# Kernel tuning notes

Hardware: AMD Instinct MI355X
Metric: run time of the kernel (lower is better)

Reference implementation:

```python
import jax, jax.numpy as jnp
import numpy as np

E = 8_388_608  # total edges across batched graphs
G = 4096       # num_graphs


def setup_inputs() -> dict:
    key = jax.random.key(0)
    k1, k2, k3 = jax.random.split(key, 3)
    edge_scores = jax.random.normal(k1, (E,), dtype=jnp.float32)
    # edge_batch: sorted segment ids in [0, G), as in PyG batched graphs
    edge_batch = jnp.sort(jax.random.randint(k2, (E,), 0, G)).astype(jnp.int32)
    candidate_mask = jax.random.bernoulli(k3, 0.5, (E,))
    return {
        "edge_scores": edge_scores,
        "edge_batch": edge_batch,
        "candidate_mask": candidate_mask,
        "num_graphs": G,
        "k": 32,
    }


def reference(edge_scores, edge_batch, candidate_mask, num_graphs, k):
    """Segmented top-k edge selection (GFlowNetActor._select_topk_candidate_edges).

    Faithful fixed-shape formulation: candidate edges come in as a boolean mask
    over all E edges (the rollout builds cand_edges = nonzero(candidate_mask)),
    and the kept top-k-per-graph edges go out as a boolean pruned mask (the
    rollout scatters the returned indices back into pruned_mask). Also returns
    the score values gated by the pruned mask (differentiable output).
    """
    n = edge_scores.shape[0]
    neg_inf = jnp.finfo(jnp.float32).min
    # Non-candidates get -inf so they sort to the back of each segment
    s = jnp.where(candidate_mask, edge_scores.astype(jnp.float32), neg_inf)
    # Sort by score descending, then stably by segment id -> within each
    # graph edges appear in descending-score order (same double-argsort as torch)
    order_score = jnp.argsort(-s, stable=True)
    order_seg = jnp.argsort(edge_batch[order_score], stable=True)
    perm = order_score[order_seg]          # [E] edge ids sorted by (seg asc, score desc)
    seg_sorted = edge_batch[perm]          # [E]
    # Segment starts via bincount + exclusive cumsum
    counts = jnp.bincount(seg_sorted, length=num_graphs)
    start = jnp.concatenate(
        [jnp.zeros(1, jnp.int32), jnp.cumsum(counts)[:-1].astype(jnp.int32)]
    )
    rank = jnp.arange(n, dtype=jnp.int32) - start[seg_sorted]
    keep_sorted = (rank < k) & candidate_mask[perm]
    # Scatter keep flags back to original edge order
    pruned_mask = jnp.zeros(n, dtype=bool).at[perm].set(keep_sorted)
    pruned_scores = jnp.where(pruned_mask, edge_scores, jnp.float32(0.0))
    return pruned_mask, pruned_scores
```

## Files before the change

kernel.cpp:

```cpp
#include <hip/hip_runtime.h>
#include <stdint.h>

#define G_NUM 4096
#define BLOCK 256
#define CAP   3072
#define ACT   1152

typedef unsigned long long ull;

__device__ __forceinline__ unsigned int order_bits(float f) {
    unsigned int b = __float_as_uint(f);
    return (b & 0x80000000u) ? ~b : (b | 0x80000000u);
}
__device__ __forceinline__ float inv_order_bits(unsigned int ob) {
    return __uint_as_float((ob & 0x80000000u) ? (ob & 0x7FFFFFFFu) : ~ob);
}

__global__ void prep_kernel(const int* __restrict__ batch, int* __restrict__ start,
                            const unsigned int* __restrict__ mraw, int* __restrict__ flag,
                            int E) {
    if (blockIdx.x == 0 && threadIdx.x < 64) {
        int lane = threadIdx.x;
        bool allI = true, allF = true;
        for (int i = lane; i < 256; i += 64) {
            unsigned int w = mraw[i];
            if (w > 1u) allI = false;
            if (w != 0u && w != 0x3F800000u) allF = false;
        }
        allI = __all(allI);
        allF = __all(allF);
        if (lane == 0) *flag = allI ? 0 : (allF ? 1 : 2);
    }
    const int n4 = E >> 2;
    int i4 = blockIdx.x * blockDim.x + threadIdx.x;
    if (i4 >= n4) return;
    int4 b = ((const int4*)batch)[i4];
    int prev = __shfl_up(b.w, 1, 64);
    if ((threadIdx.x & 63) == 0) prev = (i4 == 0) ? -1 : batch[i4 * 4 - 1];
    const int e0 = i4 * 4;
    for (int g = prev + 1; g <= b.x; ++g) start[g] = e0;
    for (int g = b.x + 1; g <= b.y; ++g) start[g] = e0 + 1;
    for (int g = b.y + 1; g <= b.z; ++g) start[g] = e0 + 2;
    for (int g = b.z + 1; g <= b.w; ++g) start[g] = e0 + 3;
    if (i4 == n4 - 1) {
        int last = b.w, e = E & ~3;
        for (int t = 0; t < (E & 3); ++t) {
            int v = batch[e + t];
            for (int g = last + 1; g <= v; ++g) start[g] = e + t;
            last = v;
        }
        for (int g = last + 1; g <= G_NUM; ++g) start[g] = E;
    }
}

__device__ __forceinline__ void scan_select(
    unsigned int* hist, unsigned int* wtot, int kk,
    int* bsel_s, unsigned int* cgt_s, unsigned int* hsel_s, int* cnt2, int tid)
{
    unsigned int h = hist[tid];
    hist[tid] = 0u;
    unsigned int v = h;
    int lane = tid & 63, wv = tid >> 6;
    #pragma unroll
    for (int off = 1; off < 64; off <<= 1) {
        unsigned int o = __shfl_down(v, off, 64);
        if (lane + off < 64) v += o;
    }
    if (lane == 0) wtot[wv] = v;
    if (tid == 0) *cnt2 = 0;
    __syncthreads();
    unsigned int sfx = v;
    for (int w = wv + 1; w < 4; ++w) sfx += wtot[w];
    if ((unsigned)kk <= sfx && (unsigned)kk > sfx - h) {
        *bsel_s = tid; *cgt_s = sfx - h; *hsel_s = h;
    }
    __syncthreads();
}

__global__ __launch_bounds__(BLOCK) void topk_kernel(
    const float* __restrict__ scores, const void* __restrict__ maskp,
    const int* __restrict__ start, const int* __restrict__ kp,
    const int* __restrict__ flagp, float* __restrict__ out_mask,
    float* __restrict__ out_scores, int E)
{
    __shared__ unsigned int keys[CAP];
    __shared__ unsigned short act[2][ACT];
    __shared__ ull candb[CAP / 64];
    __shared__ unsigned int hist[256];
    __shared__ unsigned int wtot[4];
    __shared__ int cnt, cnt2, bsel_s, licut_s;
    __shared__ unsigned int cgt_s, hsel_s, P_s;

    const int g  = blockIdx.x;
    const int s0 = start[g];
    const int s1 = start[g + 1];
    const int len = s1 - s0;
    if (len <= 0) return;

    const int k     = *kp;
    const int mflag = *flagp;
    const int tid   = threadIdx.x;
    const int lane  = tid & 63;
    const int wv    = tid >> 6;

    auto getmask = [&](int i) -> bool {
        if (mflag == 2) return ((const unsigned char*)maskp)[i] != 0;
        if (mflag == 0) return ((const int*)maskp)[i] != 0;
        return ((const float*)maskp)[i] != 0.0f;
    };

    if (k <= 0) {
        for (int i = s0 + tid; i < s1; i += BLOCK) { out_mask[i] = 0.0f; out_scores[i] = 0.0f; }
        return;
    }

    hist[tid] = 0u;
    if (tid == 0) cnt = 0;
    __syncthreads();

    if (len <= CAP) {
        const int iters = (len + BLOCK - 1) / BLOCK;
        unsigned int wcnt = 0;
        for (int it = 0; it < iters; ++it) {
            int li = it * BLOCK + tid;
            bool c = false;
            if (li < len) {
                int i = s0 + li;
                c = getmask(i);
                unsigned kb = order_bits(scores[i]);
                keys[li] = kb;
                if (c) atomicAdd(&hist[kb >> 24], 1u);
            }
            ull bal = __ballot(c);
            if (lane == 0) {
                candb[it * 4 + wv] = bal;
                wcnt += __popcll(bal);
            }
        }
        if (lane == 0 && wcnt) atomicAdd(&cnt, (int)wcnt);
        __syncthreads();
        const int m = cnt;
        const bool keep_all = (m <= k);
        unsigned int P = 0u;
        int licut = 0;

        if (!keep_all) {
            unsigned int prefix = 0u;
            int kk = k;
            int ccnt = m;
            int compacted = -1;
            int alen = 0;

            for (int shift = 24; ; shift -= 8) {
                scan_select(hist, wtot, kk, &bsel_s, &cgt_s, &hsel_s, &cnt2, tid);
                const unsigned b   = (unsigned)bsel_s;
                const unsigned cgt = cgt_s;
                const int csel     = (int)hsel_s;

                if (csel <= ACT) {
                    if (compacted < 0) {
                        for (int it = 0; it < iters; ++it) {
                            int li = it * BLOCK + tid;
                            if (li >= len) break;
                            if (!((candb[li >> 6] >> (li & 63)) & 1)) continue;
                            unsigned key = keys[li];
                            if (shift < 24 && (key >> (shift + 8)) != (prefix >> (shift + 8))) continue;
                            if (((key >> shift) & 0xFFu) == b)
                                act[0][atomicAdd(&cnt2, 1)] = (unsigned short)li;
                        }
                        compacted = 0;
                    } else {
                        int src = compacted, dst = src ^ 1;
                        for (int j = tid; j < alen; j += BLOCK) {
                            unsigned short lj = act[src][j];
                            if (((keys[lj] >> shift) & 0xFFu) == b)
                                act[dst][atomicAdd(&cnt2, 1)] = lj;
                        }
                        compacted = dst;
                    }
                    alen = csel;
                }
                prefix |= b << shift;
                kk -= (int)cgt;
                ccnt = csel;
                __syncthreads();
                if (shift == 0 || (compacted >= 0 && ccnt <= 64)) break;

                if (compacted < 0) {
                    for (int it = 0; it < iters; ++it) {
                        int li = it * BLOCK + tid;
                        if (li >= len) break;
                        if (!((candb[li >> 6] >> (li & 63)) & 1)) continue;
                        unsigned key = keys[li];
                        if ((key >> shift) == (prefix >> shift))
                            atomicAdd(&hist[(key >> (shift - 8)) & 0xFFu], 1u);
                    }
                } else {
                    for (int j = tid; j < alen; j += BLOCK)
                        atomicAdd(&hist[(keys[act[compacted][j]] >> (shift - 8)) & 0xFFu], 1u);
                }
                __syncthreads();
            }

            if (tid == 0) { P_s = prefix; licut_s = 0x7FFFFFFF; }
            __syncthreads();
            if (compacted >= 0 && ccnt <= 64) {
                if (tid < 64) {
                    unsigned key = 0u; int li = 0x7FFFFFFF;
                    if (tid < ccnt) { li = act[compacted][tid]; key = keys[li]; }
                    int r = 0;
                    for (int j = 0; j < ccnt; ++j) {
                        unsigned kj = __shfl(key, j, 64);
                        int lj = __shfl(li, j, 64);
                        if (kj > key || (kj == key && lj < li)) r++;
                    }
                    if (tid < ccnt && r == kk - 1) { P_s = key; licut_s = li; }
                }
            } else if (compacted >= 0) {
                for (int e = tid; e < alen; e += BLOCK) {
                    int li = act[compacted][e];
                    if (keys[li] != prefix) continue;
                    int r = 0;
                    for (int j = 0; j < alen; ++j) {
                        int lj = act[compacted][j];
                        if (keys[lj] == prefix && lj < li) r++;
                    }
                    if (r == kk - 1) licut_s = li;
                }
            } else {
                for (int li = tid; li < len; li += BLOCK) {
                    if (!((candb[li >> 6] >> (li & 63)) & 1)) continue;
                    if (keys[li] != prefix) continue;
                    int r = 0;
                    for (int j = 0; j < len; ++j)
                        if (((candb[j >> 6] >> (j & 63)) & 1) && keys[j] == prefix && j < li) r++;
                    if (r == kk - 1) licut_s = li;
                }
            }
            __syncthreads();
            P = P_s; licut = licut_s;
        }

        for (int it = 0; it < iters; ++it) {
            int li = it * BLOCK + tid;
            if (li >= len) break;
            bool c = (candb[li >> 6] >> (li & 63)) & 1;
            unsigned key = keys[li];
            bool kept = c && (keep_all || key > P || (key == P && li <= licut));
            out_mask[s0 + li]   = kept ? 1.0f : 0.0f;
            out_scores[s0 + li] = kept ? inv_order_bits(key) : 0.0f;
        }
    } else {
        int lc = 0;
        for (int i = s0 + tid; i < s1; i += BLOCK)
            if (getmask(i)) lc++;
        atomicAdd(&cnt, lc);
        __syncthreads();
        const int m = cnt;
        const bool keep_all = (m <= k);
        ull pivot = 0ull;
        if (!keep_all) {
            ull prefix = 0ull;
            int kk = k;
            for (int shift = 56; shift >= 0; shift -= 8) {
                for (int i = s0 + tid; i < s1; i += BLOCK) {
                    if (!getmask(i)) continue;
                    ull key = ((ull)order_bits(scores[i]) << 32) |
                              (ull)(0xFFFFFFFFu - (unsigned)(i - s0));
                    if (shift == 56 || (key >> (shift + 8)) == (prefix >> (shift + 8)))
                        atomicAdd(&hist[(unsigned)((key >> shift) & 0xFFull)], 1u);
                }
                __syncthreads();
                scan_select(hist, wtot, kk, &bsel_s, &cgt_s, &hsel_s, &cnt2, tid);
                prefix |= ((ull)(unsigned)bsel_s) << shift;
                kk -= (int)cgt_s;
            }
            pivot = prefix;
        }
        for (int i = s0 + tid; i < s1; i += BLOCK) {
            bool c = getmask(i);
            float sc = 0.0f;
            bool kept = false;
            if (c) {
                sc = scores[i];
                ull key = ((ull)order_bits(sc) << 32) |
                          (ull)(0xFFFFFFFFu - (unsigned)(i - s0));
                kept = keep_all || (key >= pivot);
            }
            out_mask[i]   = kept ? 1.0f : 0.0f;
            out_scores[i] = kept ? sc : 0.0f;
        }
    }
}

extern "C" void kernel_launch(void* const* d_in, const int* in_sizes, int n_in,
                              void* d_out, int out_size, void* d_ws, size_t ws_size,
                              hipStream_t stream) {
    const float* scores = (const float*)d_in[0];
    const int*   batch  = (const int*)d_in[1];
    const void*  mask   = d_in[2];
    const int*   kp     = (const int*)d_in[4];
    const int    E      = in_sizes[0];

    float* out_mask   = (float*)d_out;
    float* out_scores = out_mask + E;

    int* flag  = (int*)d_ws;
    int* start = (int*)((char*)d_ws + 256);

    const int n4 = E >> 2;
    prep_kernel<<<(n4 + BLOCK - 1) / BLOCK, BLOCK, 0, stream>>>(
        batch, start, (const unsigned int*)mask, flag, E);
    topk_kernel<<<G_NUM, BLOCK, 0, stream>>>(scores, mask, start, kp, flag,
                                             out_mask, out_scores, E);
}
```

Before: 52.67 us.

## Keep per-thread keys in registers with vectorized loads and small-candidate rank select

The small-segment path now has each thread own 12 contiguous edges held in registers. Scores and masks are loaded as float4/int4/uint words on interior threads, which removes the shared-memory key array and compaction buffers. The radix select stops once at most 256 candidates remain, packs them into a shared list and ranks them all-pairs, with a binary-search fallback for ties. Outputs are written with vector stores. This cuts shared-memory footprint (raising occupancy) and memory transactions, at the cost of more registers and more complex boundary handling for unaligned segment edges.

Measured after the change: 57.80 us. 9.8% more time.

```diff
diff --git a/kernel.cpp b/kernel.cpp
--- a/kernel.cpp
+++ b/kernel.cpp
@@ -3,8 +3,9 @@
 
 #define G_NUM 4096
 #define BLOCK 256
-#define CAP   3072
-#define ACT   1152
+#define VPT   12
+#define CAP   (BLOCK * VPT - 3)
+#define CLS   256
 
 typedef unsigned long long ull;
 
@@ -83,11 +84,9 @@
     const int* __restrict__ flagp, float* __restrict__ out_mask,
     float* __restrict__ out_scores, int E)
 {
-    __shared__ unsigned int keys[CAP];
-    __shared__ unsigned short act[2][ACT];
-    __shared__ ull candb[CAP / 64];
     __shared__ unsigned int hist[256];
     __shared__ unsigned int wtot[4];
+    __shared__ ull cls[CLS];
     __shared__ int cnt, cnt2, bsel_s, licut_s;
     __shared__ unsigned int cgt_s, hsel_s, P_s;
 
@@ -100,8 +99,6 @@
     const int k     = *kp;
     const int mflag = *flagp;
     const int tid   = threadIdx.x;
-    const int lane  = tid & 63;
-    const int wv    = tid >> 6;
 
     auto getmask = [&](int i) -> bool {
         if (mflag == 2) return ((const unsigned char*)maskp)[i] != 0;
@@ -116,28 +113,79 @@
 
     hist[tid] = 0u;
     if (tid == 0) cnt = 0;
-    __syncthreads();
 
     if (len <= CAP) {
-        const int iters = (len + BLOCK - 1) / BLOCK;
-        unsigned int wcnt = 0;
-        for (int it = 0; it < iters; ++it) {
-            int li = it * BLOCK + tid;
-            bool c = false;
-            if (li < len) {
-                int i = s0 + li;
-                c = getmask(i);
-                unsigned kb = order_bits(scores[i]);
-                keys[li] = kb;
-                if (c) atomicAdd(&hist[kb >> 24], 1u);
-            }
-            ull bal = __ballot(c);
-            if (lane == 0) {
-                candb[it * 4 + wv] = bal;
-                wcnt += __popcll(bal);
-            }
-        }
-        if (lane == 0 && wcnt) atomicAdd(&cnt, (int)wcnt);
+        const int a0   = s0 & ~3;
+        const int base = a0 + tid * VPT;
+        unsigned int key[VPT];
+        unsigned int candm = 0u, validm = 0u;
+        const bool interior = (base >= s0) && (base + VPT <= s1);
+
+        if (interior) {
+            validm = 0xFFFu;
+            const float4* sp = (const float4*)(scores + base);
+            #pragma unroll
+            for (int q = 0; q < 3; ++q) {
+                float4 f = sp[q];
+                key[4*q]   = order_bits(f.x);
+                key[4*q+1] = order_bits(f.y);
+                key[4*q+2] = order_bits(f.z);
+                key[4*q+3] = order_bits(f.w);
+            }
+            if (mflag == 2) {
+                const unsigned int* mp = (const unsigned int*)((const unsigned char*)maskp + base);
+                #pragma unroll
+                for (int q = 0; q < 3; ++q) {
+                    unsigned int w = mp[q];
+                    #pragma unroll
+                    for (int j = 0; j < 4; ++j)
+                        if ((w >> (8*j)) & 0xFFu) candm |= 1u << (4*q + j);
+                }
+            } else if (mflag == 0) {
+                const int4* mp = (const int4*)((const int*)maskp + base);
+                #pragma unroll
+                for (int q = 0; q < 3; ++q) {
+                    int4 w = mp[q];
+                    if (w.x) candm |= 1u << (4*q);
+                    if (w.y) candm |= 1u << (4*q + 1);
+                    if (w.z) candm |= 1u << (4*q + 2);
+                    if (w.w) candm |= 1u << (4*q + 3);
+                }
+            } else {
+                const float4* mp = (const float4*)((const float*)maskp + base);
+                #pragma unroll
+                for (int q = 0; q < 3; ++q) {
+                    float4 w = mp[q];
+                    if (w.x != 0.0f) candm |= 1u << (4*q);
+                    if (w.y != 0.0f) candm |= 1u << (4*q + 1);
+                    if (w.z != 0.0f) candm |= 1u << (4*q + 2);
+                    if (w.w != 0.0f) candm |= 1u << (4*q + 3);
+                }
+            }
+        } else if (base < s1) {
+            #pragma unroll
+            for (int v = 0; v < VPT; ++v) {
+                int gi = base + v;
+                key[v] = 0u;
+                if (gi >= s0 && gi < s1) {
+                    validm |= 1u << v;
+                    key[v] = order_bits(scores[gi]);
+                    if (getmask(gi)) candm |= 1u << v;
+                }
+            }
+        } else {
+            #pragma unroll
+            for (int v = 0; v < VPT; ++v) key[v] = 0u;
+        }
+
+        __syncthreads();
+        int lc = __popc(candm);
+        #pragma unroll
+        for (int v = 0; v < VPT; ++v)
+            if ((candm >> v) & 1u) atomicAdd(&hist[key[v] >> 24], 1u);
+        #pragma unroll
+        for (int off = 1; off < 64; off <<= 1) lc += __shfl_xor(lc, off, 64);
+        if ((tid & 63) == 0) atomicAdd(&cnt, lc);
         __syncthreads();
         const int m = cnt;
         const bool keep_all = (m <= k);
@@ -147,110 +195,101 @@
         if (!keep_all) {
             unsigned int prefix = 0u;
             int kk = k;
-            int ccnt = m;
-            int compacted = -1;
-            int alen = 0;
-
-            for (int shift = 24; ; shift -= 8) {
+            int csel = 0;
+            int shift = 24;
+            bool have_cls = false;
+            for (;;) {
                 scan_select(hist, wtot, kk, &bsel_s, &cgt_s, &hsel_s, &cnt2, tid);
-                const unsigned b   = (unsigned)bsel_s;
-                const unsigned cgt = cgt_s;
-                const int csel     = (int)hsel_s;
-
-                if (csel <= ACT) {
-                    if (compacted < 0) {
-                        for (int it = 0; it < iters; ++it) {
-                            int li = it * BLOCK + tid;
-                            if (li >= len) break;
-                            if (!((candb[li >> 6] >> (li & 63)) & 1)) continue;
-                            unsigned key = keys[li];
-                            if (shift < 24 && (key >> (shift + 8)) != (prefix >> (shift + 8))) continue;
-                            if (((key >> shift) & 0xFFu) == b)
-                                act[0][atomicAdd(&cnt2, 1)] = (unsigned short)li;
-                        }
-                        compacted = 0;
-                    } else {
-                        int src = compacted, dst = src ^ 1;
-                        for (int j = tid; j < alen; j += BLOCK) {
-                            unsigned short lj = act[src][j];
-                            if (((keys[lj] >> shift) & 0xFFu) == b)
-                                act[dst][atomicAdd(&cnt2, 1)] = lj;
-                        }
-                        compacted = dst;
+                prefix |= ((unsigned int)bsel_s) << shift;
+                kk  -= (int)cgt_s;
+                csel = (int)hsel_s;
+                if (csel <= CLS) { have_cls = true; break; }
+                if (shift == 0) break;
+                shift -= 8;
+                #pragma unroll
+                for (int v = 0; v < VPT; ++v)
+                    if (((candm >> v) & 1u) && (key[v] >> (shift + 8)) == (prefix >> (shift + 8)))
+                        atomicAdd(&hist[(key[v] >> shift) & 0xFFu], 1u);
+                __syncthreads();
+            }
+
+            if (have_cls) {
+                #pragma unroll
+                for (int v = 0; v < VPT; ++v) {
+                    if (((candm >> v) & 1u) && (key[v] >> shift) == (prefix >> shift)) {
+                        int idx = atomicAdd(&cnt2, 1);
+                        cls[idx] = ((ull)key[v] << 32) | (unsigned int)(base + v - s0);
                     }
-                    alen = csel;
-                }
-                prefix |= b << shift;
-                kk -= (int)cgt;
-                ccnt = csel;
+                }
                 __syncthreads();
-                if (shift == 0 || (compacted >= 0 && ccnt <= 64)) break;
-
-                if (compacted < 0) {
-                    for (int it = 0; it < iters; ++it) {
-                        int li = it * BLOCK + tid;
-                        if (li >= len) break;
-                        if (!((candb[li >> 6] >> (li & 63)) & 1)) continue;
-                        unsigned key = keys[li];
-                        if ((key >> shift) == (prefix >> shift))
-                            atomicAdd(&hist[(key >> (shift - 8)) & 0xFFu], 1u);
+                if (tid < csel) {
+                    ull me = cls[tid];
+                    unsigned int km = (unsigned int)(me >> 32), lm = (unsigned int)me;
+                    int r = 0;
+                    for (int j = 0; j < csel; ++j) {
+                        ull o = cls[j];
+                        unsigned int ko = (unsigned int)(o >> 32), lo = (unsigned int)o;
+                        r += (ko > km || (ko == km && lo < lm)) ? 1 : 0;
                     }
-                } else {
-                    for (int j = tid; j < alen; j += BLOCK)
-                        atomicAdd(&hist[(keys[act[compacted][j]] >> (shift - 8)) & 0xFFu], 1u);
+                    if (r == kk - 1) { P_s = km; licut_s = (int)lm; }
                 }
                 __syncthreads();
-            }
-
-            if (tid == 0) { P_s = prefix; licut_s = 0x7FFFFFFF; }
-            __syncthreads();
-            if (compacted >= 0 && ccnt <= 64) {
-                if (tid < 64) {
-                    unsigned key = 0u; int li = 0x7FFFFFFF;
-                    if (tid < ccnt) { li = act[compacted][tid]; key = keys[li]; }
-                    int r = 0;
-                    for (int j = 0; j < ccnt; ++j) {
-                        unsigned kj = __shfl(key, j, 64);
-                        int lj = __shfl(li, j, 64);
-                        if (kj > key || (kj == key && lj < li)) r++;
-                    }
-                    if (tid < ccnt && r == kk - 1) { P_s = key; licut_s = li; }
-                }
-            } else if (compacted >= 0) {
-                for (int e = tid; e < alen; e += BLOCK) {
-                    int li = act[compacted][e];
-                    if (keys[li] != prefix) continue;
-                    int r = 0;
-                    for (int j = 0; j < alen; ++j) {
-                        int lj = act[compacted][j];
-                        if (keys[lj] == prefix && lj < li) r++;
-                    }
-                    if (r == kk - 1) licut_s = li;
-                }
+                P = P_s; licut = licut_s;
             } else {
-                for (int li = tid; li < len; li += BLOCK) {
-                    if (!((candb[li >> 6] >> (li & 63)) & 1)) continue;
-                    if (keys[li] != prefix) continue;
-                    int r = 0;
-                    for (int j = 0; j < len; ++j)
-                        if (((candb[j >> 6] >> (j & 63)) & 1) && keys[j] == prefix && j < li) r++;
-                    if (r == kk - 1) licut_s = li;
-                }
-            }
-            __syncthreads();
-            P = P_s; licut = licut_s;
-        }
-
-        for (int it = 0; it < iters; ++it) {
-            int li = it * BLOCK + tid;
-            if (li >= len) break;
-            bool c = (candb[li >> 6] >> (li & 63)) & 1;
-            unsigned key = keys[li];
-            bool kept = c && (keep_all || key > P || (key == P && li <= licut));
-            out_mask[s0 + li]   = kept ? 1.0f : 0.0f;
-            out_scores[s0 + li] = kept ? inv_order_bits(key) : 0.0f;
+                P = prefix;
+                int lo = 0, hi = len - 1;
+                while (lo < hi) {
+                    int mid = (lo + hi) >> 1;
+                    if (tid == 0) cnt2 = 0;
+                    __syncthreads();
+                    int c = 0;
+                    #pragma unroll
+                    for (int v = 0; v < VPT; ++v)
+                        if (((candm >> v) & 1u) && key[v] == prefix && (base + v - s0) <= mid) c++;
+                    #pragma unroll
+                    for (int off = 1; off < 64; off <<= 1) c += __shfl_xor(c, off, 64);
+                    if ((tid & 63) == 0) atomicAdd(&cnt2, c);
+                    __syncthreads();
+                    int total = cnt2;
+                    __syncthreads();
+                    if (total >= kk) hi = mid; else lo = mid + 1;
+                }
+                licut = lo;
+            }
+        }
+
+        if (interior) {
+            #pragma unroll
+            for (int q = 0; q < 3; ++q) {
+                float4 vm, vs;
+                float* pm = (float*)&vm;
+                float* ps = (float*)&vs;
+                #pragma unroll
+                for (int j = 0; j < 4; ++j) {
+                    int v = 4*q + j;
+                    int li = base + v - s0;
+                    bool kept = ((candm >> v) & 1u) &&
+                        (keep_all || key[v] > P || (key[v] == P && li <= licut));
+                    pm[j] = kept ? 1.0f : 0.0f;
+                    ps[j] = kept ? inv_order_bits(key[v]) : 0.0f;
+                }
+                *(float4*)(out_mask   + base + 4*q) = vm;
+                *(float4*)(out_scores + base + 4*q) = vs;
+            }
+        } else if (base < s1) {
+            #pragma unroll
+            for (int v = 0; v < VPT; ++v) {
+                int gi = base + v;
+                if (gi < s0 || gi >= s1) continue;
+                int li = gi - s0;
+                bool kept = ((candm >> v) & 1u) &&
+                    (keep_all || key[v] > P || (key[v] == P && li <= licut));
+                out_mask[gi]   = kept ? 1.0f : 0.0f;
+                out_scores[gi] = kept ? inv_order_bits(key[v]) : 0.0f;
+            }
         }
     } else {
+        __syncthreads();
         int lc = 0;
         for (int i = s0 + tid; i < s1; i += BLOCK)
             if (getmask(i)) lc++;
```
